# Optimization experiments

Measured on AMD Instinct MI355X. Metric: run time of the kernel, lower is better.

Reference implementation:

```python
import jax, jax.numpy as jnp
import numpy as np
from jax import lax

V, E, H, MEL = 256, 512, 1024, 128
B, T_TXT, T_MEL = 128, 256, 800
BN_EPS = 1e-5


def setup_inputs() -> dict:
    key = jax.random.key(0)
    ks = jax.random.split(key, 32)
    s = 0.05
    n = jax.random.normal
    inp = {
        "x": jax.random.randint(ks[0], (B, T_TXT), 0, V),
        "text_seq_lens": jax.random.randint(ks[1], (B,), 1, T_TXT + 1),
        "y": n(ks[2], (B, T_MEL, MEL), jnp.float32),
        "mel_spec_lens": jax.random.randint(ks[3], (B,), 1, T_MEL + 1),
        # encoder params
        "emb": n(ks[4], (V, E)) * s,
        "enc_lin_W": n(ks[5], (E, E)) * s,
        "enc_lin_b": jnp.zeros((E,)),
        "conv1_W": n(ks[6], (E, E, 3)) * s,
        "conv1_b": jnp.zeros((E,)),
        "bn1_g": 1.0 + n(ks[7], (E,)) * s,
        "bn1_b": n(ks[8], (E,)) * s,
        "conv2_W": n(ks[9], (E, E, 3)) * s,
        "conv2_b": jnp.zeros((E,)),
        "bn2_g": 1.0 + n(ks[10], (E,)) * s,
        "bn2_b": n(ks[11], (E,)) * s,
        # encoder LSTM (torch gate order i,f,g,o); b = b_ih + b_hh fused
        "Wih_e": n(ks[12], (4 * H, E)) * s,
        "Whh_e": n(ks[13], (4 * H, H)) * s,
        "b_e": n(ks[14], (4 * H,)) * 0.01,
        # decoder LSTM
        "Wih_d": n(ks[15], (4 * H, MEL)) * s,
        "Whh_d": n(ks[16], (4 * H, H)) * s,
        "b_d": n(ks[17], (4 * H,)) * 0.01,
        # output projections
        "Wp": n(ks[18], (MEL, H)) * s,
        "bp": jnp.zeros((MEL,)),
        "Wg": n(ks[19], (1, H)) * s,
        "bg": jnp.zeros((1,)),
    }
    return inp


def lstm_step(xt, h, c, Wih, Whh, b):
    g = xt @ Wih.T + h @ Whh.T + b  # [B, 4H]
    i, f, gg, o = jnp.split(g, 4, axis=-1)
    c2 = jax.nn.sigmoid(f) * c + jax.nn.sigmoid(i) * jnp.tanh(gg)
    h2 = jax.nn.sigmoid(o) * jnp.tanh(c2)
    return h2, c2


def reference(x, text_seq_lens, y, mel_spec_lens, emb, enc_lin_W, enc_lin_b,
              conv1_W, conv1_b, bn1_g, bn1_b, conv2_W, conv2_b, bn2_g, bn2_b,
              Wih_e, Whh_e, b_e, Wih_d, Whh_d, b_d, Wp, bp, Wg, bg):
    Bq, Ttxt = x.shape
    Tmel = y.shape[1]
    dt = y.dtype

    def conv_bn_relu(h, W, b, g, beta):
        h = lax.conv_general_dilated(h, W, (1,), ((1, 1),),
                                     dimension_numbers=("NCH", "OIH", "NCH"))
        h = h + b[None, :, None]
        # BN in eval mode: running_mean=0, running_var=1
        h = g[None, :, None] * (h / jnp.sqrt(1.0 + BN_EPS)) + beta[None, :, None]
        return jax.nn.relu(h)  # dropout is identity in eval

    e = emb[x]                                  # [B,T,E]
    e = e @ enc_lin_W.T + enc_lin_b
    h = e.transpose(0, 2, 1)                    # [B,E,T]
    h = conv_bn_relu(h, conv1_W, conv1_b, bn1_g, bn1_b)
    h = conv_bn_relu(h, conv2_W, conv2_b, bn2_g, bn2_b)
    h = h.transpose(0, 2, 1)                    # [B,T,E]

    # encoder LSTM with pack_padded semantics: state frozen past seq len,
    # so final (h,c) is the state at each sequence's true last step.
    valid = jnp.arange(Ttxt)[:, None] < text_seq_lens[None, :]  # [T,B]

    def enc_step(carry, inp):
        hh, cc = carry
        xt, v = inp
        h2, c2 = lstm_step(xt, hh, cc, Wih_e, Whh_e, b_e)
        v = v[:, None]
        return (jnp.where(v, h2, hh), jnp.where(v, c2, cc)), None

    z = jnp.zeros((Bq, H), dt)
    (hS, cS), _ = lax.scan(enc_step, (z, z), (h.transpose(1, 0, 2), valid))

    def dec_step(carry, _):
        hh, cc, inp = carry
        h2, c2 = lstm_step(inp, hh, cc, Wih_d, Whh_d, b_d)
        mel = h2 @ Wp.T + bp           # [B,MEL]
        gate = (h2 @ Wg.T + bg)[:, 0]  # [B]
        return (h2, c2, mel), (mel, gate)

    sos = jnp.zeros((Bq, MEL), dt)
    _, (mels, gates) = lax.scan(dec_step, (hS, cS, sos), None, length=Tmel)
    mels = mels.transpose(1, 0, 2)   # [B,Tmel,MEL]
    gates = gates.T                  # [B,Tmel]

    mask = jnp.arange(Tmel)[None, :] > mel_spec_lens[:, None]  # strict > as in source
    masked_mel = jnp.where(mask[:, :, None], jnp.zeros((), dt), mels)
    masked_gate = jnp.where(mask, jnp.asarray(1000.0, dt), gates)
    return masked_mel, masked_gate, mask
```

## Files before the change

### kernel.cpp

```cpp
#include <hip/hip_runtime.h>
#include <math.h>

#define BB 128
#define TT 256
#define TMEL 800
#define EE 512
#define HH 1024
#define MELD 128
#define VV 256

#define OFF_PROJ  0u
#define OFF_T1    131072u
#define OFF_WR2   524288u
#define OFF_BB1   1310720u
#define OFF_BB2   1311232u
#define OFF_B2    1311744u
#define OFF_W2C   1315840u
#define OFF_BAR   5510144u
#define OFF_WENCR 5522688u
#define OFF_WIHS  7619840u
#define OFF_W2CR  8668416u
#define OFF_WHHDS 10765568u
#define OFF_WPGS  12862720u
#define OFF_H2B   12936448u
#define OFF_RING  21325056u

typedef __bf16 bfv8 __attribute__((ext_vector_type(8)));
typedef float f32x4 __attribute__((ext_vector_type(4)));

__device__ __forceinline__ unsigned short f2b(float f){
  union { float f; unsigned u; } v; v.f = f;
  unsigned u = v.u;
  return (unsigned short)((u + 0x7fffu + ((u>>16)&1u)) >> 16);
}
__device__ __forceinline__ float sigm(float x){ return 1.0f/(1.0f+expf(-x)); }

__device__ __forceinline__ f32x4 mfma16(bfv8 a, bfv8 b, f32x4 c){
  return __builtin_amdgcn_mfma_f32_16x16x32_bf16(a, b, c, 0, 0, 0);
}


__global__ void k_proj(const float* __restrict__ emb, const float* __restrict__ W,
                       const float* __restrict__ bias, float* __restrict__ proj){
  __shared__ float er[EE];
  int v = blockIdx.x;
  for(int i=threadIdx.x;i<EE;i+=256) er[i]=emb[v*EE+i];
  __syncthreads();
  for(int e=threadIdx.x;e<EE;e+=256){
    const float* wr = W + e*EE;
    float acc=0.f;
    for(int k=0;k<EE;k+=4){
      float4 w4 = *(const float4*)(wr+k);
      acc += er[k]*w4.x + er[k+1]*w4.y + er[k+2]*w4.z + er[k+3]*w4.w;
    }
    proj[v*EE+e] = acc + bias[e];
  }
}

__global__ void k_t1(const float* __restrict__ proj, const float* __restrict__ W1,
                     const float* __restrict__ g1, float* __restrict__ T1){
  __shared__ float pr[EE];
  int v = blockIdx.x; int k3 = blockIdx.y;
  for(int i=threadIdx.x;i<EE;i+=256) pr[i]=proj[v*EE+i];
  __syncthreads();
  const float s = rsqrtf(1.f+1e-5f);
  for(int c=threadIdx.x;c<EE;c+=256){
    float acc=0.f;
    const float* w = W1 + c*EE*3 + k3;
    for(int ci=0;ci<EE;ci++) acc += pr[ci]*w[ci*3];
    T1[(v*3+k3)*EE+c] = g1[c]*s*acc;
  }
}

__global__ void k_wr2(const float* __restrict__ W2, const float* __restrict__ g2,
                      unsigned short* __restrict__ Wr){
  int idx = blockIdx.x*256+threadIdx.x;
  if(idx >= EE*3*EE) return;
  int c = idx/1536; int r = idx%1536; int k3 = r/EE; int ci = r%EE;
  const float s = rsqrtf(1.f+1e-5f);
  Wr[idx] = f2b(g2[c]*s*W2[(c*EE+ci)*3+k3]);
}

__global__ void k_bb(const float* __restrict__ b1,const float* __restrict__ g1,const float* __restrict__ be1,
                     const float* __restrict__ b2,const float* __restrict__ g2,const float* __restrict__ be2,
                     float* __restrict__ bb1, float* __restrict__ bb2){
  int c = threadIdx.x + blockIdx.x*256; if(c>=EE) return;
  const float s = rsqrtf(1.f+1e-5f);
  bb1[c] = g1[c]*s*b1[c] + be1[c];
  bb2[c] = g2[c]*s*b2[c] + be2[c];
}

__global__ void k_b2(const float* __restrict__ bd, const float* __restrict__ Wih,
                     const float* __restrict__ bp, float* __restrict__ b2){
  int j = blockIdx.x*256+threadIdx.x; if(j>=4096) return;
  float acc = bd[j];
  const float* w = Wih + j*MELD;
  for(int m=0;m<MELD;m++) acc += w[m]*bp[m];
  b2[j] = acc;
}

__global__ void k_w2c(const float* __restrict__ Whh, const float* __restrict__ Wih,
                      const float* __restrict__ Wp, float* __restrict__ W2c){
  __shared__ float wl[8][MELD];
  int j0 = blockIdx.x*8; int k = blockIdx.y*256 + threadIdx.x;
  for(int i=threadIdx.x;i<8*MELD;i+=256) wl[i/MELD][i%MELD] = Wih[(j0+i/MELD)*MELD + (i%MELD)];
  __syncthreads();
  float acc[8];
  #pragma unroll
  for(int jj=0;jj<8;jj++) acc[jj]=Whh[(j0+jj)*HH+k];
  for(int m=0;m<MELD;m++){
    float wp = Wp[m*HH+k];
    #pragma unroll
    for(int jj=0;jj<8;jj++) acc[jj] += wl[jj][m]*wp;
  }
  #pragma unroll
  for(int jj=0;jj<8;jj++) W2c[(j0+jj)*HH+k] = acc[jj];
}

__global__ void k_pack(const float* __restrict__ src, unsigned short* __restrict__ dst,
                       int NKT, int K){
  int tile = blockIdx.x;
  int cg = tile>>3, wv = tile&7;
  int tot = NKT*64*8;
  for(int i=threadIdx.x; i<tot; i+=256){
    int kt = i>>9; int l = (i>>3)&63; int e = i&7;
    int j = (wv>>1)*1024 + cg*32 + (wv&1)*16 + (l&15);
    int k = ((l>>4)<<3) + kt*32 + e;
    dst[((size_t)(tile*NKT + kt)*64 + l)*8 + e] = f2b(src[(size_t)j*K + k]);
  }
}

__global__ void k_pack_pg(const float* __restrict__ Wp, const float* __restrict__ Wg,
                          unsigned short* __restrict__ dst){
  int nt = blockIdx.x;
  for(int i=threadIdx.x; i<32*64*8; i+=256){
    int kt = i>>9; int l = (i>>3)&63; int e = i&7;
    int n = nt*16 + (l&15);
    int k = ((l>>4)<<3) + kt*32 + e;
    float v = (n<MELD)? Wp[(size_t)n*HH+k] : (n==MELD? Wg[k] : 0.f);
    dst[((size_t)(nt*32 + kt)*64 + l)*8 + e] = f2b(v);
  }
}


__global__ void k_pad(unsigned short* __restrict__ h1pb){
  int idx = blockIdx.x*256+threadIdx.x;
  int c = idx & 511; int b = idx >> 9;
  h1pb[((size_t)b*258)*EE + c] = 0;
  h1pb[((size_t)b*258 + 257)*EE + c] = 0;
}

__global__ void k_conv1(const int* __restrict__ x, const float* __restrict__ T1,
                        const float* __restrict__ bb1, unsigned short* __restrict__ h1pb){
  int idx = blockIdx.x*256+threadIdx.x;
  int c = idx & 511; int bt = idx >> 9; int t = bt & 255; int b = bt >> 8;
  float acc = bb1[c];
  if(t > 0)    acc += T1[(size_t)(x[b*TT+t-1]*3+0)*EE+c];
               acc += T1[(size_t)(x[b*TT+t  ]*3+1)*EE+c];
  if(t < TT-1) acc += T1[(size_t)(x[b*TT+t+1]*3+2)*EE+c];
  h1pb[((size_t)b*258 + t + 1)*EE + c] = f2b(fmaxf(acc, 0.f));
}

template<int NKT>
__device__ __forceinline__ void mm_seg_stream(const unsigned short* A, int lda,
    const unsigned short* Wrow, f32x4& acc0, f32x4& acc1, int l, int wv){
  int r0 = wv*32 + (l&15);
  int k8 = (l>>4)*8;
  const unsigned short* a0 = A + (size_t)r0*lda + k8;
  const unsigned short* a1 = a0 + 16*lda;
  const unsigned short* wp = Wrow + k8;
  #pragma unroll
  for(int kt=0;kt<NKT;kt++){
    bfv8 bv = *(const bfv8*)(const void*)(wp + kt*32);
    acc0 = mfma16(*(const bfv8*)(const void*)(a0 + kt*32), bv, acc0);
    acc1 = mfma16(*(const bfv8*)(const void*)(a1 + kt*32), bv, acc1);
  }
}

__global__ __launch_bounds__(256,2) void k_conv2mm(const unsigned short* __restrict__ h1pb,
    const unsigned short* __restrict__ Wr2b, const float* __restrict__ bb2,
    unsigned short* __restrict__ h2b){
  int b = blockIdx.x;
  int th = blockIdx.y;
  int nt = blockIdx.z;
  int tid=threadIdx.x; int wv=tid>>6, l=tid&63;
  const unsigned short* A = h1pb + ((size_t)b*258 + th*128)*EE;
  const unsigned short* Wrow = Wr2b + (size_t)(nt*16+(l&15))*1536;
  f32x4 acc0={0,0,0,0}, acc1={0,0,0,0};
  mm_seg_stream<48>(A, EE, Wrow, acc0, acc1, l, wv);
  int rr=(l>>4)*4, cc=l&15;
  int n = nt*16+cc;
  float bias = bb2[n];
  #pragma unroll
  for(int mi=0;mi<2;mi++){
    f32x4 acc = mi?acc1:acc0;
    int tb = th*128 + wv*32 + mi*16 + rr;
    #pragma unroll
    for(int q=0;q<4;q++){
      float v = fmaxf(acc[q]+bias, 0.f);
      h2b[((size_t)(tb+q)*BB + b)*EE + n] = f2b(v);
    }
  }
}

__device__ __forceinline__ void g_arrive(unsigned int* cnt, unsigned int* gen){
  __syncthreads();
  if(threadIdx.x == 0){
    unsigned int old = __hip_atomic_fetch_add(cnt, 1u, __ATOMIC_RELAXED, __HIP_MEMORY_SCOPE_AGENT);
    if(old == 31u){
      __hip_atomic_store(cnt, 0u, __ATOMIC_RELAXED, __HIP_MEMORY_SCOPE_AGENT);
      __hip_atomic_fetch_add(gen, 1u, __ATOMIC_RELAXED, __HIP_MEMORY_SCOPE_AGENT);
    }
  }
}
__device__ __forceinline__ void g_wait(unsigned int* gen, unsigned int target){
  if(threadIdx.x == 0){
    while(__hip_atomic_load(gen, __ATOMIC_RELAXED, __HIP_MEMORY_SCOPE_AGENT) < target)
      __builtin_amdgcn_s_sleep(1);
  }
  asm volatile("" ::: "memory");
  __syncthreads();
}

__device__ __forceinline__ void stage_h(unsigned short* hs, const unsigned short* slotp,
                                        int bg, int tid){
  for(int i = tid; i < 4096; i += 512){
    int r = i >> 8, c8 = i & 255;
    const unsigned long long* p =
      (const unsigned long long*)(slotp + (size_t)(bg*16+r)*HH + c8*4);
    unsigned long long v = __hip_atomic_load(p, __ATOMIC_RELAXED, __HIP_MEMORY_SCOPE_AGENT);
    *(unsigned long long*)((char*)hs + ((r*2048 + c8*8) ^ ((r&7)<<4))) = v;
  }
}

__global__ __launch_bounds__(512,1) void k_recur(
  const unsigned short* __restrict__ h2b, unsigned short* __restrict__ ring,
  const unsigned short* __restrict__ WencR, const unsigned short* __restrict__ WihS,
  const unsigned short* __restrict__ W2cR, const unsigned short* __restrict__ WhhdS,
  const unsigned short* __restrict__ WpgS,
  const float* __restrict__ bhe, const float* __restrict__ bd, const float* __restrict__ b2,
  const float* __restrict__ bp, const float* __restrict__ bgp,
  unsigned int* __restrict__ bar,
  const int* __restrict__ tlen, const int* __restrict__ mlen,
  float* __restrict__ outmel, float* __restrict__ outgate)
{
  __shared__ __align__(16) unsigned short hs[16*1024];
  __shared__ __align__(16) unsigned short Xs[16*512];
  __shared__ float Gs[16][132];

  const int bid = blockIdx.x;
  const int bg = bid >> 5, cg = bid & 31;
  const int tid = threadIdx.x;
  const int wvi = tid >> 6, l = tid & 63;
  const int tile = cg*8 + wvi;
  unsigned int* cnt = bar + bg*32;
  unsigned int* gen = bar + 256 + bg*32;
  unsigned int ge = 1;

  const int fr = l & 15;
  const int hswz = (fr & 7) << 4;
  const int hbase = fr*2048 + ((l>>4)<<4);
  const int xbase = fr*1024 + ((l>>4)<<4);

  const int lr = tid >> 4;
  const int lc = (tid & 15) * 2;
  const int hcol = cg*32 + lc;
  float cs0 = 0.f, cs1 = 0.f;
  unsigned int hp = 0u;
  int mylen = 0;
  if(tid < 256) mylen = tlen[bg*16 + lr];

  if(tid < 128){
    int r = tid >> 3, c4 = (tid & 7) * 4;
    unsigned long long* p = (unsigned long long*)
      (ring + (size_t)100*BB*HH + (size_t)(bg*16+r)*HH + cg*32 + c4);
    __hip_atomic_store(p, 0ull, __ATOMIC_RELAXED, __HIP_MEMORY_SCOPE_AGENT);
  }
  g_arrive(cnt, gen);

  f32x4 bw[32];

  {
    const f32x4* wsrc = (const f32x4*)(const void*)(WencR + ((size_t)(tile*32)*64 + l)*8);
    #pragma unroll
    for(int kt=0;kt<32;kt++) bw[kt] = wsrc[kt*64];
    #pragma unroll
    for(int kt=0;kt<32;kt++) asm volatile("" : "+v"(bw[kt]));
  }

  float ei0=0,ei1=0,ef0=0,ef1=0,eg0=0,eg1=0,eo0=0,eo1=0;
  if(tid < 256){
    ei0=bhe[hcol];      ei1=bhe[hcol+1];
    ef0=bhe[HH+hcol];   ef1=bhe[HH+hcol+1];
    eg0=bhe[2*HH+hcol]; eg1=bhe[2*HH+hcol+1];
    eo0=bhe[3*HH+hcol]; eo1=bhe[3*HH+hcol+1];
  }

  #pragma unroll 1
  for(int t=0;t<TT;t++){
    {
      const uint4* src = (const uint4*)(h2b + (size_t)(t*BB + bg*16)*EE);
      for(int i = tid; i < 1024; i += 512){
        int r = i >> 6, c16 = i & 63;
        uint4 v = src[r*64 + c16];
        *(uint4*)((char*)Xs + ((r*1024 + c16*16) ^ ((r&7)<<4))) = v;
      }
    }
    __syncthreads();
    f32x4 acc = {0.f,0.f,0.f,0.f};
    {
      const unsigned short* wsrc = WihS + (size_t)tile*16*64*8;
      #pragma unroll
      for(int kt=0;kt<16;kt++){
        bfv8 wf = *(const bfv8*)(const void*)(wsrc + ((size_t)kt*64 + l)*8);
        bfv8 xv = *(const bfv8*)(const void*)((const char*)Xs + ((xbase + kt*64) ^ hswz));
        acc = mfma16(xv, wf, acc);
      }
    }
    g_wait(gen, ge);
    stage_h(hs, ring + (size_t)(100 + (t&1))*BB*HH, bg, tid);
    __syncthreads();
    #pragma unroll
    for(int kt=0;kt<32;kt++){
      bfv8 hv = *(const bfv8*)(const void*)((const char*)hs + ((hbase + kt*64) ^ hswz));
      acc = mfma16(hv, __builtin_bit_cast(bfv8, bw[kt]), acc);
    }
    {
      int rr = (l>>4)*4;
      #pragma unroll
      for(int q=0;q<4;q++) Gs[rr+q][wvi*16 + fr] = acc[q];
    }
    __syncthreads();
    if(tid < 256){
      float gi0 = Gs[lr][lc]    + ei0, gi1 = Gs[lr][lc+1] + ei1;
      float gf0 = Gs[lr][32+lc] + ef0, gf1 = Gs[lr][33+lc] + ef1;
      float gg0 = Gs[lr][64+lc] + eg0, gg1 = Gs[lr][65+lc] + eg1;
      float go0 = Gs[lr][96+lc] + eo0, go1 = Gs[lr][97+lc] + eo1;
      float c20 = sigm(gf0)*cs0 + sigm(gi0)*tanhf(gg0);
      float c21 = sigm(gf1)*cs1 + sigm(gi1)*tanhf(gg1);
      float h20 = sigm(go0)*tanhf(c20);
      float h21 = sigm(go1)*tanhf(c21);
      if(t < mylen){
        cs0 = c20; cs1 = c21;
        hp = (unsigned)f2b(h20) | ((unsigned)f2b(h21)<<16);
      }
      unsigned short* outslot = (t==TT-1) ? (ring + (size_t)99*BB*HH)
                                          : (ring + (size_t)(100 + ((t+1)&1))*BB*HH);
      __hip_atomic_store((unsigned int*)(outslot + (size_t)(bg*16+lr)*HH + hcol), hp,
                         __ATOMIC_RELAXED, __HIP_MEMORY_SCOPE_AGENT);
    }
    g_arrive(cnt, gen); ge++;
  }

  {
    const f32x4* wsrc = (const f32x4*)(const void*)(W2cR + ((size_t)(tile*32)*64 + l)*8);
    #pragma unroll
    for(int kt=0;kt<32;kt++) bw[kt] = wsrc[kt*64];
    #pragma unroll
    for(int kt=0;kt<32;kt++) asm volatile("" : "+v"(bw[kt]));
  }

  float di0=0,di1=0,df0=0,df1=0,dg0=0,dg1=0,do0=0,do1=0;
  if(tid < 256){
    di0=b2[hcol];      di1=b2[hcol+1];
    df0=b2[HH+hcol];   df1=b2[HH+hcol+1];
    dg0=b2[2*HH+hcol]; dg1=b2[2*HH+hcol+1];
    do0=b2[3*HH+hcol]; do1=b2[3*HH+hcol+1];
  }

  #pragma unroll 1
  for(int t=0;t<TMEL;t++){
    g_wait(gen, ge);
    const unsigned short* slotin = (t==0) ? ring + (size_t)99*BB*HH
                                          : ring + (size_t)((t-1)%100)*BB*HH;
    stage_h(hs, slotin, bg, tid);
    __syncthreads();
    f32x4 acc = {0.f,0.f,0.f,0.f};
    if(t == 0){
      const unsigned short* wsrc = WhhdS + (size_t)tile*32*64*8;
      #pragma unroll
      for(int kt=0;kt<32;kt++){
        bfv8 wf = *(const bfv8*)(const void*)(wsrc + ((size_t)kt*64 + l)*8);
        bfv8 hv = *(const bfv8*)(const void*)((const char*)hs + ((hbase + kt*64) ^ hswz));
        acc = mfma16(hv, wf, acc);
      }
    } else {
      #pragma unroll
      for(int kt=0;kt<32;kt++){
        bfv8 hv = *(const bfv8*)(const void*)((const char*)hs + ((hbase + kt*64) ^ hswz));
        acc = mfma16(hv, __builtin_bit_cast(bfv8, bw[kt]), acc);
      }
    }
    {
      int rr = (l>>4)*4;
      #pragma unroll
      for(int q=0;q<4;q++) Gs[rr+q][wvi*16 + fr] = acc[q];
    }
    __syncthreads();
    if(tid < 256){
      float bi0=di0,bi1=di1,bf0=df0,bf1=df1,bg0=dg0,bg1=dg1,bo0=do0,bo1=do1;
      if(t==0){
        bi0=bd[hcol];      bi1=bd[hcol+1];
        bf0=bd[HH+hcol];   bf1=bd[HH+hcol+1];
        bg0=bd[2*HH+hcol]; bg1=bd[2*HH+hcol+1];
        bo0=bd[3*HH+hcol]; bo1=bd[3*HH+hcol+1];
      }
      float gi0 = Gs[lr][lc]    + bi0, gi1 = Gs[lr][lc+1] + bi1;
      float gf0 = Gs[lr][32+lc] + bf0, gf1 = Gs[lr][33+lc] + bf1;
      float gg0 = Gs[lr][64+lc] + bg0, gg1 = Gs[lr][65+lc] + bg1;
      float go0 = Gs[lr][96+lc] + bo0, go1 = Gs[lr][97+lc] + bo1;
      float c20 = sigm(gf0)*cs0 + sigm(gi0)*tanhf(gg0);
      float c21 = sigm(gf1)*cs1 + sigm(gi1)*tanhf(gg1);
      cs0 = c20; cs1 = c21;
      float h20 = sigm(go0)*tanhf(c20);
      float h21 = sigm(go1)*tanhf(c21);
      unsigned int hn = (unsigned)f2b(h20) | ((unsigned)f2b(h21)<<16);
      unsigned short* outslot = ring + (size_t)(t%100)*BB*HH;
      __hip_atomic_store((unsigned int*)(outslot + (size_t)(bg*16+lr)*HH + hcol), hn,
                         __ATOMIC_RELAXED, __HIP_MEMORY_SCOPE_AGENT);
    }
    g_arrive(cnt, gen); ge++;

    if((t%100)==99){
      g_wait(gen, ge);
      int tbase = t - 99;
      #pragma unroll 1
      for(int s = cg; s < 100; s += 32){
        stage_h(hs, ring + (size_t)s*BB*HH, bg, tid);
        __syncthreads();
        int tout = tbase + s;
        #pragma unroll 1
        for(int pass=0; pass<2; pass++){
          int nt = (pass==0) ? wvi : 8;
          if(pass==1 && wvi!=0) break;
          const unsigned short* wsrc = WpgS + (size_t)nt*32*64*8;
          f32x4 acc = {0.f,0.f,0.f,0.f};
          #pragma unroll
          for(int kt=0;kt<32;kt++){
            bfv8 wf = *(const bfv8*)(const void*)(wsrc + ((size_t)kt*64 + l)*8);
            bfv8 hv = *(const bfv8*)(const void*)((const char*)hs + ((hbase + kt*64) ^ hswz));
            acc = mfma16(hv, wf, acc);
          }
          int n = nt*16 + fr;
          #pragma unroll
          for(int q=0;q<4;q++){
            int b = bg*16 + (l>>4)*4 + q;
            bool msk = tout > mlen[b];
            if(n < MELD)
              outmel[((size_t)b*TMEL + tout)*MELD + n] = msk ? 0.f : acc[q]+bp[n];
            else if(n == MELD)
              outgate[(size_t)b*TMEL + tout] = msk ? 1000.f : acc[q]+bgp[0];
          }
        }
        __syncthreads();
      }
      g_arrive(cnt, gen); ge++;
    }
  }
}

__global__ void k_mask(const int* __restrict__ mlen, float* __restrict__ om){
  int idx=blockIdx.x*256+threadIdx.x; if(idx>=BB*TMEL) return;
  int b=idx/TMEL, t=idx%TMEL;
  om[idx] = (t > mlen[b]) ? 1.f : 0.f;
}

extern "C" void kernel_launch(void* const* d_in, const int* in_sizes, int n_in,
                              void* d_out, int out_size, void* d_ws, size_t ws_size,
                              hipStream_t stream){
  (void)in_sizes; (void)n_in; (void)out_size; (void)ws_size;
  const int*   x    = (const int*)d_in[0];
  const int*   tlen = (const int*)d_in[1];
  const int*   mlen = (const int*)d_in[3];
  const float* emb  = (const float*)d_in[4];
  const float* elW  = (const float*)d_in[5];
  const float* elb  = (const float*)d_in[6];
  const float* c1W  = (const float*)d_in[7];
  const float* c1b  = (const float*)d_in[8];
  const float* g1   = (const float*)d_in[9];
  const float* be1  = (const float*)d_in[10];
  const float* c2W  = (const float*)d_in[11];
  const float* c2b  = (const float*)d_in[12];
  const float* g2   = (const float*)d_in[13];
  const float* be2  = (const float*)d_in[14];
  const float* Wihe = (const float*)d_in[15];
  const float* Whhe = (const float*)d_in[16];
  const float* bhe  = (const float*)d_in[17];
  const float* Wihd = (const float*)d_in[18];
  const float* Whhd = (const float*)d_in[19];
  const float* bhd  = (const float*)d_in[20];
  const float* Wp   = (const float*)d_in[21];
  const float* bp   = (const float*)d_in[22];
  const float* Wg   = (const float*)d_in[23];
  const float* bg   = (const float*)d_in[24];

  float* ws = (float*)d_ws;
  float* proj = ws + OFF_PROJ;
  float* T1   = ws + OFF_T1;
  unsigned short* Wr2b = (unsigned short*)(ws + OFF_WR2);
  float* bb1 = ws + OFF_BB1;
  float* bb2 = ws + OFF_BB2;
  float* b2  = ws + OFF_B2;
  float* W2c = ws + OFF_W2C;
  unsigned int* bar = (unsigned int*)(ws + OFF_BAR);
  unsigned short* WencR = (unsigned short*)(ws + OFF_WENCR);
  unsigned short* WihS  = (unsigned short*)(ws + OFF_WIHS);
  unsigned short* W2cR  = (unsigned short*)(ws + OFF_W2CR);
  unsigned short* WhhdS = (unsigned short*)(ws + OFF_WHHDS);
  unsigned short* WpgS  = (unsigned short*)(ws + OFF_WPGS);
  unsigned short* h2b   = (unsigned short*)(ws + OFF_H2B);
  unsigned short* h1pb  = (unsigned short*)(ws + OFF_RING);
  unsigned short* ring  = (unsigned short*)(ws + OFF_RING);

  float* outmel  = (float*)d_out;
  float* outgate = outmel + (size_t)BB*TMEL*MELD;
  float* outmask = outgate + (size_t)BB*TMEL;

  hipMemsetAsync(bar, 0, 2048, stream);

  k_proj<<<VV,256,0,stream>>>(emb, elW, elb, proj);
  k_t1<<<dim3(VV,3),256,0,stream>>>(proj, c1W, g1, T1);
  k_wr2<<<(EE*3*EE+255)/256,256,0,stream>>>(c2W, g2, Wr2b);
  k_bb<<<2,256,0,stream>>>(c1b,g1,be1,c2b,g2,be2,bb1,bb2);
  k_b2<<<16,256,0,stream>>>(bhd, Wihd, bp, b2);
  k_w2c<<<dim3(4096/8,HH/256),256,0,stream>>>(Whhd, Wihd, Wp, W2c);
  k_pack<<<256,256,0,stream>>>(Whhe, WencR, 32, 1024);
  k_pack<<<256,256,0,stream>>>(Wihe, WihS, 16, 512);
  k_pack<<<256,256,0,stream>>>(W2c,  W2cR, 32, 1024);
  k_pack<<<256,256,0,stream>>>(Whhd, WhhdS, 32, 1024);
  k_pack_pg<<<9,256,0,stream>>>(Wp, Wg, WpgS);
  k_pad<<<256,256,0,stream>>>(h1pb);
  k_conv1<<<65536,256,0,stream>>>(x, T1, bb1, h1pb);
  k_conv2mm<<<dim3(BB,2,32),256,0,stream>>>(h1pb, Wr2b, bb2, h2b);

  void* kargs[] = {
    (void*)&h2b, (void*)&ring, (void*)&WencR, (void*)&WihS, (void*)&W2cR, (void*)&WhhdS,
    (void*)&WpgS, (void*)&bhe, (void*)&bhd, (void*)&b2, (void*)&bp, (void*)&bg,
    (void*)&bar, (void*)&tlen, (void*)&mlen, (void*)&outmel, (void*)&outgate
  };
  hipLaunchCooperativeKernel((void*)k_recur, dim3(256), dim3(512), kargs, 0u, stream);

  k_mask<<<(BB*TMEL+255)/256,256,0,stream>>>(mlen, outmask);
}
```

Measured before the change: 9.225 ms.

## Replace counter-based group barrier with per-block flag array and split MFMA accumulators

The group barrier no longer uses a shared atomic counter plus a generation word. Each block now stores its generation number into its own flag slot, and waiters poll all 32 flags in parallel with 32 threads. This removes the serialized atomic fetch-add and the second hop through the generation counter on every recurrent step. Separately, the MFMA reduction chains are split into two independent accumulators that are summed at the end, shortening the dependency chain. This relies on the barrier flag memory being zero-initialized, and it adds more polling traffic.

```diff
diff --git a/kernel.cpp b/kernel.cpp
--- a/kernel.cpp
+++ b/kernel.cpp
@@ -203,19 +203,14 @@
   }
 }
 
-__device__ __forceinline__ void g_arrive(unsigned int* cnt, unsigned int* gen){
+__device__ __forceinline__ void g_arrive(unsigned int* frow, int cg, unsigned int ge){
   __syncthreads();
-  if(threadIdx.x == 0){
-    unsigned int old = __hip_atomic_fetch_add(cnt, 1u, __ATOMIC_RELAXED, __HIP_MEMORY_SCOPE_AGENT);
-    if(old == 31u){
-      __hip_atomic_store(cnt, 0u, __ATOMIC_RELAXED, __HIP_MEMORY_SCOPE_AGENT);
-      __hip_atomic_fetch_add(gen, 1u, __ATOMIC_RELAXED, __HIP_MEMORY_SCOPE_AGENT);
-    }
-  }
-}
-__device__ __forceinline__ void g_wait(unsigned int* gen, unsigned int target){
-  if(threadIdx.x == 0){
-    while(__hip_atomic_load(gen, __ATOMIC_RELAXED, __HIP_MEMORY_SCOPE_AGENT) < target)
+  if(threadIdx.x == 0)
+    __hip_atomic_store(frow + cg, ge, __ATOMIC_RELAXED, __HIP_MEMORY_SCOPE_AGENT);
+}
+__device__ __forceinline__ void g_wait(unsigned int* frow, unsigned int ge){
+  if(threadIdx.x < 32){
+    while(__hip_atomic_load(frow + threadIdx.x, __ATOMIC_RELAXED, __HIP_MEMORY_SCOPE_AGENT) < ge)
       __builtin_amdgcn_s_sleep(1);
   }
   asm volatile("" ::: "memory");
@@ -253,9 +248,8 @@
   const int tid = threadIdx.x;
   const int wvi = tid >> 6, l = tid & 63;
   const int tile = cg*8 + wvi;
-  unsigned int* cnt = bar + bg*32;
-  unsigned int* gen = bar + 256 + bg*32;
-  unsigned int ge = 1;
+  unsigned int* frow = bar + bg*32;
+  unsigned int ge = 0;
 
   const int fr = l & 15;
   const int hswz = (fr & 7) << 4;
@@ -276,7 +270,7 @@
       (ring + (size_t)100*BB*HH + (size_t)(bg*16+r)*HH + cg*32 + c4);
     __hip_atomic_store(p, 0ull, __ATOMIC_RELAXED, __HIP_MEMORY_SCOPE_AGENT);
   }
-  g_arrive(cnt, gen);
+  ge++; g_arrive(frow, cg, ge);
 
   f32x4 bw[32];
 
@@ -307,25 +301,31 @@
       }
     }
     __syncthreads();
-    f32x4 acc = {0.f,0.f,0.f,0.f};
+    f32x4 a0 = {0.f,0.f,0.f,0.f}, a1 = {0.f,0.f,0.f,0.f};
     {
       const unsigned short* wsrc = WihS + (size_t)tile*16*64*8;
       #pragma unroll
-      for(int kt=0;kt<16;kt++){
-        bfv8 wf = *(const bfv8*)(const void*)(wsrc + ((size_t)kt*64 + l)*8);
-        bfv8 xv = *(const bfv8*)(const void*)((const char*)Xs + ((xbase + kt*64) ^ hswz));
-        acc = mfma16(xv, wf, acc);
-      }
-    }
-    g_wait(gen, ge);
+      for(int kt=0;kt<16;kt+=2){
+        bfv8 wf0 = *(const bfv8*)(const void*)(wsrc + ((size_t)kt*64 + l)*8);
+        bfv8 wf1 = *(const bfv8*)(const void*)(wsrc + ((size_t)(kt+1)*64 + l)*8);
+        bfv8 xv0 = *(const bfv8*)(const void*)((const char*)Xs + ((xbase + kt*64) ^ hswz));
+        bfv8 xv1 = *(const bfv8*)(const void*)((const char*)Xs + ((xbase + (kt+1)*64) ^ hswz));
+        a0 = mfma16(xv0, wf0, a0);
+        a1 = mfma16(xv1, wf1, a1);
+      }
+    }
+    g_wait(frow, ge);
     stage_h(hs, ring + (size_t)(100 + (t&1))*BB*HH, bg, tid);
     __syncthreads();
     #pragma unroll
-    for(int kt=0;kt<32;kt++){
-      bfv8 hv = *(const bfv8*)(const void*)((const char*)hs + ((hbase + kt*64) ^ hswz));
-      acc = mfma16(hv, __builtin_bit_cast(bfv8, bw[kt]), acc);
+    for(int kt=0;kt<32;kt+=2){
+      bfv8 hv0 = *(const bfv8*)(const void*)((const char*)hs + ((hbase + kt*64) ^ hswz));
+      bfv8 hv1 = *(const bfv8*)(const void*)((const char*)hs + ((hbase + (kt+1)*64) ^ hswz));
+      a0 = mfma16(hv0, __builtin_bit_cast(bfv8, bw[kt]), a0);
+      a1 = mfma16(hv1, __builtin_bit_cast(bfv8, bw[kt+1]), a1);
     }
     {
+      f32x4 acc = a0 + a1;
       int rr = (l>>4)*4;
       #pragma unroll
       for(int q=0;q<4;q++) Gs[rr+q][wvi*16 + fr] = acc[q];
@@ -349,7 +349,7 @@
       __hip_atomic_store((unsigned int*)(outslot + (size_t)(bg*16+lr)*HH + hcol), hp,
                          __ATOMIC_RELAXED, __HIP_MEMORY_SCOPE_AGENT);
     }
-    g_arrive(cnt, gen); ge++;
+    ge++; g_arrive(frow, cg, ge);
   }
 
   {
@@ -370,28 +370,34 @@
 
   #pragma unroll 1
   for(int t=0;t<TMEL;t++){
-    g_wait(gen, ge);
+    g_wait(frow, ge);
     const unsigned short* slotin = (t==0) ? ring + (size_t)99*BB*HH
                                           : ring + (size_t)((t-1)%100)*BB*HH;
     stage_h(hs, slotin, bg, tid);
     __syncthreads();
-    f32x4 acc = {0.f,0.f,0.f,0.f};
+    f32x4 a0 = {0.f,0.f,0.f,0.f}, a1 = {0.f,0.f,0.f,0.f};
     if(t == 0){
       const unsigned short* wsrc = WhhdS + (size_t)tile*32*64*8;
       #pragma unroll
-      for(int kt=0;kt<32;kt++){
-        bfv8 wf = *(const bfv8*)(const void*)(wsrc + ((size_t)kt*64 + l)*8);
-        bfv8 hv = *(const bfv8*)(const void*)((const char*)hs + ((hbase + kt*64) ^ hswz));
-        acc = mfma16(hv, wf, acc);
+      for(int kt=0;kt<32;kt+=2){
+        bfv8 wf0 = *(const bfv8*)(const void*)(wsrc + ((size_t)kt*64 + l)*8);
+        bfv8 wf1 = *(const bfv8*)(const void*)(wsrc + ((size_t)(kt+1)*64 + l)*8);
+        bfv8 hv0 = *(const bfv8*)(const void*)((const char*)hs + ((hbase + kt*64) ^ hswz));
+        bfv8 hv1 = *(const bfv8*)(const void*)((const char*)hs + ((hbase + (kt+1)*64) ^ hswz));
+        a0 = mfma16(hv0, wf0, a0);
+        a1 = mfma16(hv1, wf1, a1);
       }
     } else {
       #pragma unroll
-      for(int kt=0;kt<32;kt++){
-        bfv8 hv = *(const bfv8*)(const void*)((const char*)hs + ((hbase + kt*64) ^ hswz));
-        acc = mfma16(hv, __builtin_bit_cast(bfv8, bw[kt]), acc);
+      for(int kt=0;kt<32;kt+=2){
+        bfv8 hv0 = *(const bfv8*)(const void*)((const char*)hs + ((hbase + kt*64) ^ hswz));
+        bfv8 hv1 = *(const bfv8*)(const void*)((const char*)hs + ((hbase + (kt+1)*64) ^ hswz));
+        a0 = mfma16(hv0, __builtin_bit_cast(bfv8, bw[kt]), a0);
+        a1 = mfma16(hv1, __builtin_bit_cast(bfv8, bw[kt+1]), a1);
       }
     }
     {
+      f32x4 acc = a0 + a1;
       int rr = (l>>4)*4;
       #pragma unroll
       for(int q=0;q<4;q++) Gs[rr+q][wvi*16 + fr] = acc[q];
@@ -419,10 +425,10 @@
       __hip_atomic_store((unsigned int*)(outslot + (size_t)(bg*16+lr)*HH + hcol), hn,
                          __ATOMIC_RELAXED, __HIP_MEMORY_SCOPE_AGENT);
     }
-    g_arrive(cnt, gen); ge++;
+    ge++; g_arrive(frow, cg, ge);
 
     if((t%100)==99){
-      g_wait(gen, ge);
+      g_wait(frow, ge);
       int tbase = t - 99;
       #pragma unroll 1
       for(int s = cg; s < 100; s += 32){
@@ -454,7 +460,7 @@
         }
         __syncthreads();
       }
-      g_arrive(cnt, gen); ge++;
+      ge++; g_arrive(frow, cg, ge);
     }
   }
 }
```

Measured after the change: 10.39 ms. +12.7%, slower.

## Replace group barriers with per-element tag-bit flags embedded in hidden-state ring

Applied to the files above, without the earlier changes.

Removes the atomic counter/generation barrier between the 32 blocks of each batch group. Instead, the low bit of every packed bf16 pair carries a parity tag, and consumers spin on the data words themselves until the tag matches. The encoder uses a 3-slot ring and the decoder a 101-slot ring so tags alternate safely, and the ring is pre-filled with memsets. This cuts per-step barrier latency, at the cost of perturbing one mantissa bit of each hidden value and adding memset traffic and more fragile ordering assumptions.

```diff
diff --git a/kernel.cpp b/kernel.cpp
--- a/kernel.cpp
+++ b/kernel.cpp
@@ -16,7 +16,6 @@
 #define OFF_BB2   1311232u
 #define OFF_B2    1311744u
 #define OFF_W2C   1315840u
-#define OFF_BAR   5510144u
 #define OFF_WENCR 5522688u
 #define OFF_WIHS  7619840u
 #define OFF_W2CR  8668416u
@@ -203,33 +202,30 @@
   }
 }
 
-__device__ __forceinline__ void g_arrive(unsigned int* cnt, unsigned int* gen){
-  __syncthreads();
-  if(threadIdx.x == 0){
-    unsigned int old = __hip_atomic_fetch_add(cnt, 1u, __ATOMIC_RELAXED, __HIP_MEMORY_SCOPE_AGENT);
-    if(old == 31u){
-      __hip_atomic_store(cnt, 0u, __ATOMIC_RELAXED, __HIP_MEMORY_SCOPE_AGENT);
-      __hip_atomic_fetch_add(gen, 1u, __ATOMIC_RELAXED, __HIP_MEMORY_SCOPE_AGENT);
-    }
-  }
-}
-__device__ __forceinline__ void g_wait(unsigned int* gen, unsigned int target){
-  if(threadIdx.x == 0){
-    while(__hip_atomic_load(gen, __ATOMIC_RELAXED, __HIP_MEMORY_SCOPE_AGENT) < target)
+__device__ __forceinline__ void stage_wait(unsigned short* hs, const unsigned short* slotp,
+                                           int bg, int tid, unsigned int tagbit){
+  const unsigned long long tagpat = (unsigned long long)tagbit * 0x0000000100000001ull;
+  const unsigned long long* p[8];
+  unsigned long long v[8];
+  #pragma unroll
+  for(int j=0;j<8;j++){
+    int i = tid + j*512;
+    int r = i >> 8, c8 = i & 255;
+    p[j] = (const unsigned long long*)(slotp + (size_t)(bg*16+r)*HH + c8*4);
+    v[j] = __hip_atomic_load(p[j], __ATOMIC_RELAXED, __HIP_MEMORY_SCOPE_AGENT);
+  }
+  #pragma unroll
+  for(int j=0;j<8;j++){
+    while(((v[j] ^ tagpat) & 0x0000000100000001ull) != 0ull){
       __builtin_amdgcn_s_sleep(1);
-  }
-  asm volatile("" ::: "memory");
-  __syncthreads();
-}
-
-__device__ __forceinline__ void stage_h(unsigned short* hs, const unsigned short* slotp,
-                                        int bg, int tid){
-  for(int i = tid; i < 4096; i += 512){
+      v[j] = __hip_atomic_load(p[j], __ATOMIC_RELAXED, __HIP_MEMORY_SCOPE_AGENT);
+    }
+  }
+  #pragma unroll
+  for(int j=0;j<8;j++){
+    int i = tid + j*512;
     int r = i >> 8, c8 = i & 255;
-    const unsigned long long* p =
-      (const unsigned long long*)(slotp + (size_t)(bg*16+r)*HH + c8*4);
-    unsigned long long v = __hip_atomic_load(p, __ATOMIC_RELAXED, __HIP_MEMORY_SCOPE_AGENT);
-    *(unsigned long long*)((char*)hs + ((r*2048 + c8*8) ^ ((r&7)<<4))) = v;
+    *(unsigned long long*)((char*)hs + ((r*2048 + c8*8) ^ ((r&7)<<4))) = v[j];
   }
 }
 
@@ -240,7 +236,6 @@
   const unsigned short* __restrict__ WpgS,
   const float* __restrict__ bhe, const float* __restrict__ bd, const float* __restrict__ b2,
   const float* __restrict__ bp, const float* __restrict__ bgp,
-  unsigned int* __restrict__ bar,
   const int* __restrict__ tlen, const int* __restrict__ mlen,
   float* __restrict__ outmel, float* __restrict__ outgate)
 {
@@ -253,9 +248,7 @@
   const int tid = threadIdx.x;
   const int wvi = tid >> 6, l = tid & 63;
   const int tile = cg*8 + wvi;
-  unsigned int* cnt = bar + bg*32;
-  unsigned int* gen = bar + 256 + bg*32;
-  unsigned int ge = 1;
+  unsigned short* const encbase = ring + (size_t)101*BB*HH;
 
   const int fr = l & 15;
   const int hswz = (fr & 7) << 4;
@@ -269,14 +262,6 @@
   unsigned int hp = 0u;
   int mylen = 0;
   if(tid < 256) mylen = tlen[bg*16 + lr];
-
-  if(tid < 128){
-    int r = tid >> 3, c4 = (tid & 7) * 4;
-    unsigned long long* p = (unsigned long long*)
-      (ring + (size_t)100*BB*HH + (size_t)(bg*16+r)*HH + cg*32 + c4);
-    __hip_atomic_store(p, 0ull, __ATOMIC_RELAXED, __HIP_MEMORY_SCOPE_AGENT);
-  }
-  g_arrive(cnt, gen);
 
   f32x4 bw[32];
 
@@ -317,8 +302,7 @@
         acc = mfma16(xv, wf, acc);
       }
     }
-    g_wait(gen, ge);
-    stage_h(hs, ring + (size_t)(100 + (t&1))*BB*HH, bg, tid);
+    stage_wait(hs, encbase + (size_t)(t%3)*BB*HH, bg, tid, (unsigned)((t/3)&1));
     __syncthreads();
     #pragma unroll
     for(int kt=0;kt<32;kt++){
@@ -344,12 +328,12 @@
         cs0 = c20; cs1 = c21;
         hp = (unsigned)f2b(h20) | ((unsigned)f2b(h21)<<16);
       }
-      unsigned short* outslot = (t==TT-1) ? (ring + (size_t)99*BB*HH)
-                                          : (ring + (size_t)(100 + ((t+1)&1))*BB*HH);
-      __hip_atomic_store((unsigned int*)(outslot + (size_t)(bg*16+lr)*HH + hcol), hp,
+      unsigned int wtag = (unsigned)(((t+1)/3)&1);
+      unsigned short* outslot = encbase + (size_t)((t+1)%3)*BB*HH;
+      __hip_atomic_store((unsigned int*)(outslot + (size_t)(bg*16+lr)*HH + hcol),
+                         (hp & ~1u) | wtag,
                          __ATOMIC_RELAXED, __HIP_MEMORY_SCOPE_AGENT);
     }
-    g_arrive(cnt, gen); ge++;
   }
 
   {
@@ -370,10 +354,11 @@
 
   #pragma unroll 1
   for(int t=0;t<TMEL;t++){
-    g_wait(gen, ge);
-    const unsigned short* slotin = (t==0) ? ring + (size_t)99*BB*HH
-                                          : ring + (size_t)((t-1)%100)*BB*HH;
-    stage_h(hs, slotin, bg, tid);
+    const unsigned short* slotin;
+    unsigned int ctag;
+    if(t == 0){ slotin = encbase + (size_t)(TT%3)*BB*HH; ctag = (unsigned)((TT/3)&1); }
+    else      { slotin = ring + (size_t)((t-1)%101)*BB*HH; ctag = (unsigned)(((t-1)/101)&1); }
+    stage_wait(hs, slotin, bg, tid, ctag);
     __syncthreads();
     f32x4 acc = {0.f,0.f,0.f,0.f};
     if(t == 0){
@@ -414,47 +399,46 @@
       cs0 = c20; cs1 = c21;
       float h20 = sigm(go0)*tanhf(c20);
       float h21 = sigm(go1)*tanhf(c21);
-      unsigned int hn = (unsigned)f2b(h20) | ((unsigned)f2b(h21)<<16);
-      unsigned short* outslot = ring + (size_t)(t%100)*BB*HH;
-      __hip_atomic_store((unsigned int*)(outslot + (size_t)(bg*16+lr)*HH + hcol), hn,
+      unsigned int pk = (unsigned)f2b(h20) | ((unsigned)f2b(h21)<<16);
+      unsigned int wtag = (unsigned)((t/101)&1);
+      unsigned short* outslot = ring + (size_t)(t%101)*BB*HH;
+      __hip_atomic_store((unsigned int*)(outslot + (size_t)(bg*16+lr)*HH + hcol),
+                         (pk & ~1u) | wtag,
                          __ATOMIC_RELAXED, __HIP_MEMORY_SCOPE_AGENT);
     }
-    g_arrive(cnt, gen); ge++;
 
     if((t%100)==99){
-      g_wait(gen, ge);
       int tbase = t - 99;
       #pragma unroll 1
       for(int s = cg; s < 100; s += 32){
-        stage_h(hs, ring + (size_t)s*BB*HH, bg, tid);
+        int u = tbase + s;
+        stage_wait(hs, ring + (size_t)(u%101)*BB*HH, bg, tid, (unsigned)((u/101)&1));
         __syncthreads();
-        int tout = tbase + s;
         #pragma unroll 1
         for(int pass=0; pass<2; pass++){
           int nt = (pass==0) ? wvi : 8;
           if(pass==1 && wvi!=0) break;
           const unsigned short* wsrc = WpgS + (size_t)nt*32*64*8;
-          f32x4 acc = {0.f,0.f,0.f,0.f};
+          f32x4 acc2 = {0.f,0.f,0.f,0.f};
           #pragma unroll
           for(int kt=0;kt<32;kt++){
             bfv8 wf = *(const bfv8*)(const void*)(wsrc + ((size_t)kt*64 + l)*8);
             bfv8 hv = *(const bfv8*)(const void*)((const char*)hs + ((hbase + kt*64) ^ hswz));
-            acc = mfma16(hv, wf, acc);
+            acc2 = mfma16(hv, wf, acc2);
           }
           int n = nt*16 + fr;
           #pragma unroll
           for(int q=0;q<4;q++){
             int b = bg*16 + (l>>4)*4 + q;
-            bool msk = tout > mlen[b];
+            bool msk = u > mlen[b];
             if(n < MELD)
-              outmel[((size_t)b*TMEL + tout)*MELD + n] = msk ? 0.f : acc[q]+bp[n];
+              outmel[((size_t)b*TMEL + u)*MELD + n] = msk ? 0.f : acc2[q]+bp[n];
             else if(n == MELD)
-              outgate[(size_t)b*TMEL + tout] = msk ? 1000.f : acc[q]+bgp[0];
+              outgate[(size_t)b*TMEL + u] = msk ? 1000.f : acc2[q]+bgp[0];
           }
         }
         __syncthreads();
       }
-      g_arrive(cnt, gen); ge++;
     }
   }
 }
@@ -502,7 +486,6 @@
   float* bb2 = ws + OFF_BB2;
   float* b2  = ws + OFF_B2;
   float* W2c = ws + OFF_W2C;
-  unsigned int* bar = (unsigned int*)(ws + OFF_BAR);
   unsigned short* WencR = (unsigned short*)(ws + OFF_WENCR);
   unsigned short* WihS  = (unsigned short*)(ws + OFF_WIHS);
   unsigned short* W2cR  = (unsigned short*)(ws + OFF_W2CR);
@@ -515,8 +498,6 @@
   float* outmel  = (float*)d_out;
   float* outgate = outmel + (size_t)BB*TMEL*MELD;
   float* outmask = outgate + (size_t)BB*TMEL;
-
-  hipMemsetAsync(bar, 0, 2048, stream);
 
   k_proj<<<VV,256,0,stream>>>(emb, elW, elb, proj);
   k_t1<<<dim3(VV,3),256,0,stream>>>(proj, c1W, g1, T1);
@@ -533,10 +514,14 @@
   k_conv1<<<65536,256,0,stream>>>(x, T1, bb1, h1pb);
   k_conv2mm<<<dim3(BB,2,32),256,0,stream>>>(h1pb, Wr2b, bb2, h2b);
 
+  hipMemsetAsync(ring, 0x01, (size_t)101*BB*HH*2, stream);
+  hipMemsetAsync(ring + (size_t)101*BB*HH, 0x00, (size_t)BB*HH*2, stream);
+  hipMemsetAsync(ring + (size_t)102*BB*HH, 0x01, (size_t)2*BB*HH*2, stream);
+
   void* kargs[] = {
     (void*)&h2b, (void*)&ring, (void*)&WencR, (void*)&WihS, (void*)&W2cR, (void*)&WhhdS,
     (void*)&WpgS, (void*)&bhe, (void*)&bhd, (void*)&b2, (void*)&bp, (void*)&bg,
-    (void*)&bar, (void*)&tlen, (void*)&mlen, (void*)&outmel, (void*)&outgate
+    (void*)&tlen, (void*)&mlen, (void*)&outmel, (void*)&outgate
   };
   hipLaunchCooperativeKernel((void*)k_recur, dim3(256), dim3(512), kargs, 0u, stream);
 
```

Result: slower. 10.46 ms (+13.4%).
